# Kernel tuning notes

Measured on AMD Instinct MI355X. Metric: run time of the kernel, lower is better.

The kernel has to match this reference:

```python
import jax, jax.numpy as jnp
import numpy as np

B, T, L = 64, 256, 20
WV, WD = 100000, 300
CV, CD = 100, 100
PV, PD = 50, 100
NF, K = 100, 3
H = 256
D0 = WD + PD + NF        # 500, layer-0 LSTM input
D1 = 2 * H               # 512, later layers' input


def _lstm_dir(gx, mask, w_hh, reverse):
    # gx: [B,T,4H] precomputed input contribution + bias; mask: [B,T,1]
    if reverse:
        gx = gx[:, ::-1]
        mask = mask[:, ::-1]
    b, h = gx.shape[0], w_hh.shape[1]
    h0 = jnp.zeros((b, h), gx.dtype)

    def step(carry, xs):
        hp, cp = carry
        g_t, m_t = xs
        gates = g_t + hp @ w_hh.T
        i, f, g, o = jnp.split(gates, 4, axis=-1)
        i = jax.nn.sigmoid(i); f = jax.nn.sigmoid(f)
        o = jax.nn.sigmoid(o); g = jnp.tanh(g)
        c_new = f * cp + i * g
        h_new = o * jnp.tanh(c_new)
        hn = m_t * h_new + (1.0 - m_t) * hp   # masked step (pad positions keep state)
        cn = m_t * c_new + (1.0 - m_t) * cp
        return (hn, cn), hn

    _, hs = jax.lax.scan(step, (h0, h0), (gx.transpose(1, 0, 2), mask.transpose(1, 0, 2)))
    hs = hs.transpose(1, 0, 2)
    return hs[:, ::-1] if reverse else hs


def _bilstm_layer(x, mask, w_ih, w_hh, b):
    # w_ih: [2,4H,D], w_hh: [2,4H,H], b: [2,4H] (b_ih+b_hh combined)
    outs = []
    for d in range(2):
        gx = jnp.einsum('btd,gd->btg', x, w_ih[d]) + b[d]
        outs.append(_lstm_dir(gx, mask, w_hh[d], reverse=(d == 1)))
    return jnp.concatenate(outs, axis=-1)


def setup_inputs() -> dict:
    key = jax.random.key(0)
    ks = jax.random.split(key, 16)
    s = 0.05
    inp = {
        'input_word': jax.random.randint(ks[0], (B, T), 0, WV),
        'input_char': jax.random.randint(ks[1], (B, T, L), 0, CV),
        'input_pos': jax.random.randint(ks[2], (B, T), 0, PV),
        'mask': jnp.ones((B, T), jnp.float32),
        'emb_word': jax.random.normal(ks[3], (WV, WD), jnp.float32) * s,
        'emb_char': jax.random.normal(ks[4], (CV, CD), jnp.float32) * s,
        'emb_pos': jax.random.normal(ks[5], (PV, PD), jnp.float32) * s,
        'conv_w': jax.random.normal(ks[6], (NF, CD, K), jnp.float32) * s,
        'conv_b': jax.random.normal(ks[7], (NF,), jnp.float32) * s,
        'w_ih0': jax.random.normal(ks[8], (2, 4 * H, D0), jnp.float32) * s,
        'w_hh0': jax.random.normal(ks[9], (2, 4 * H, H), jnp.float32) * s,
        'b0': jax.random.normal(ks[10], (2, 4 * H), jnp.float32) * s,
        'w_ih1': jax.random.normal(ks[11], (2, 4 * H, D1), jnp.float32) * s,
        'w_hh1': jax.random.normal(ks[12], (2, 4 * H, H), jnp.float32) * s,
        'b1': jax.random.normal(ks[13], (2, 4 * H), jnp.float32) * s,
        'w_ih2': jax.random.normal(ks[14], (2, 4 * H, D1), jnp.float32) * s,
        'w_hh2': jax.random.normal(ks[15], (2, 4 * H, H), jnp.float32) * s,
        'b2': jax.random.normal(jax.random.fold_in(key, 99), (2, 4 * H), jnp.float32) * s,
    }
    return inp


def reference(input_word, input_char, input_pos, mask,
              emb_word, emb_char, emb_pos, conv_w, conv_b,
              w_ih0, w_hh0, b0, w_ih1, w_hh1, b1, w_ih2, w_hh2, b2):
    # dropout layers are identity in eval mode
    word = emb_word[input_word]                       # [B,T,WD]
    b, t, l = input_char.shape
    ch = emb_char[input_char].reshape(b * t, l, CD).transpose(0, 2, 1)  # [BT,CD,L]
    conv = jax.lax.conv_general_dilated(
        ch, conv_w, window_strides=(1,), padding=[(K - 1, K - 1)],
        dimension_numbers=('NCH', 'OIH', 'NCH')) + conv_b[None, :, None]
    ch = jnp.tanh(conv.max(axis=2)).reshape(b, t, NF)  # [B,T,NF]
    pos = emb_pos[input_pos]                           # [B,T,PD]
    x = jnp.concatenate([word, ch, pos], axis=-1)      # [B,T,D0]
    m = mask[..., None]
    x = _bilstm_layer(x, m, w_ih0, w_hh0, b0)
    x = _bilstm_layer(x, m, w_ih1, w_hh1, b1)
    x = _bilstm_layer(x, m, w_ih2, w_hh2, b2)
    return x                                           # [B,T,2H]
```

## Files before the change

kernel.cpp:

```cpp
#include <hip/hip_runtime.h>
#include <cstdint>
#include <cstddef>
#include <type_traits>
#include <utility>

typedef unsigned short u16;
typedef short short8 __attribute__((ext_vector_type(8)));
typedef __bf16 bf16x8 __attribute__((ext_vector_type(8)));
typedef float float4v __attribute__((ext_vector_type(4)));

__device__ __forceinline__ float bf2f(u16 u) {
  union { uint32_t i; float f; } v; v.i = ((uint32_t)u) << 16; return v.f;
}
__device__ __forceinline__ u16 f2bf(float f) {
  union { uint32_t i; float f; } v; v.f = f;
  uint32_t u = v.i;
  return (u16)((u + 0x7FFFu + ((u >> 16) & 1u)) >> 16);
}

__device__ __forceinline__ float fsig(float x) {
  float e = __expf(-x);
  return __builtin_amdgcn_rcpf(1.0f + e);
}
__device__ __forceinline__ float ftanh(float x) {
  float e = __expf(2.0f * x);
  return 1.0f - 2.0f * __builtin_amdgcn_rcpf(e + 1.0f);
}

__device__ __forceinline__ void bar_lgkm() {
  __builtin_amdgcn_sched_barrier(0);
  asm volatile("s_waitcnt lgkmcnt(0)" ::: "memory");
  __builtin_amdgcn_s_barrier();
  __builtin_amdgcn_sched_barrier(0);
}
__device__ __forceinline__ void bar_only() {
  __builtin_amdgcn_sched_barrier(0);
  __builtin_amdgcn_s_barrier();
  __builtin_amdgcn_sched_barrier(0);
}
__device__ __forceinline__ void bar_vm4() {
  __builtin_amdgcn_sched_barrier(0);
  asm volatile("s_waitcnt vmcnt(4) lgkmcnt(0)" ::: "memory");
  __builtin_amdgcn_s_barrier();
  __builtin_amdgcn_sched_barrier(0);
}

template <class V, class = void> struct MfmaTakesShort : std::false_type {};
template <class V>
struct MfmaTakesShort<V, std::void_t<decltype(__builtin_amdgcn_mfma_f32_16x16x32_bf16(
    std::declval<V>(), std::declval<V>(), std::declval<float4v>(), 0, 0, 0))>>
    : std::true_type {};

template <bool UseShort> struct MF {
  template <class V>
  static __device__ __forceinline__ float4v run(V a, V b, float4v c) {
    return __builtin_amdgcn_mfma_f32_16x16x32_bf16(a, b, c, 0, 0, 0);
  }
};
template <> struct MF<false> {
  template <class V>
  static __device__ __forceinline__ float4v run(V a, V b, float4v c) {
    return __builtin_amdgcn_mfma_f32_16x16x32_bf16(
        __builtin_bit_cast(bf16x8, a), __builtin_bit_cast(bf16x8, b), c, 0, 0, 0);
  }
};
__device__ __forceinline__ float4v mfma_bf16(short8 a, short8 b, float4v c) {
  return MF<MfmaTakesShort<short8>::value>::run(a, b, c);
}

__global__ void k_cvt_wih(const float* __restrict__ w, u16* __restrict__ o, int Kin) {
  int id = blockIdx.x * 256 + threadIdx.x;
  int n = id >> 9, k = id & 511;
  o[id] = (k < Kin) ? f2bf(w[(long)n * Kin + k]) : (u16)0;
}

__global__ void k_cvt_whh(const float* __restrict__ w, u16* __restrict__ o) {
  int id = blockIdx.x * 256 + threadIdx.x;
  o[id] = f2bf(w[id]);
}

__global__ void k_proj(const float* __restrict__ ec, const float* __restrict__ cw,
                       u16* __restrict__ proj) {
  int v = blockIdx.x, idx = threadIdx.x;
  if (idx >= 300) return;
  int k = idx / 100, nf = idx % 100;
  float s = 0.f;
  for (int cd = 0; cd < 100; cd++)
    s += ec[v * 100 + cd] * cw[(nf * 100 + cd) * 3 + k];
  proj[v * 300 + k * 100 + nf] = f2bf(s);
}

__global__ void k_embed(const int* __restrict__ iw, const int* __restrict__ ip,
                        const float* __restrict__ ew, const float* __restrict__ ep,
                        u16* __restrict__ x) {
  int row = blockIdx.x, j = threadIdx.x;
  u16 v;
  if (j < 300) v = f2bf(ew[(long)iw[row] * 300 + j]);
  else if (j < 400) return;
  else if (j < 500) v = f2bf(ep[ip[row] * 100 + (j - 400)]);
  else v = 0;
  x[row * 512 + j] = v;
}

__global__ __launch_bounds__(128) void k_charconv(const int* __restrict__ ic,
                                                  const u16* __restrict__ proj,
                                                  const float* __restrict__ cb,
                                                  u16* __restrict__ x) {
  __shared__ u16 pl[30000];
  __shared__ int ids[20];
  int tid = threadIdx.x;
  for (int i = tid; i < 15000; i += 128)
    ((uint32_t*)pl)[i] = ((const uint32_t*)proj)[i];
  float bias = (tid < 100) ? cb[tid] : 0.f;
  for (int r = 0; r < 16; r++) {
    int row = blockIdx.x * 16 + r;
    __syncthreads();
    if (tid < 20) ids[tid] = ic[row * 20 + tid];
    __syncthreads();
    if (tid < 100) {
      float mx = -1e30f;
      for (int p = 0; p < 22; p++) {
        float s = 0.f;
#pragma unroll
        for (int k = 0; k < 3; k++) {
          int q = p + k - 2;
          if (q >= 0 && q < 20) s += bf2f(pl[ids[q] * 300 + k * 100 + tid]);
        }
        mx = fmaxf(mx, s);
      }
      x[row * 512 + 300 + tid] = f2bf(ftanh(mx + bias));
    }
  }
}

template <bool GXF32>
__global__ __launch_bounds__(256) void k_gemm(const u16* __restrict__ A,
                                              const u16* __restrict__ Bm,
                                              const float* __restrict__ bias,
                                              void* __restrict__ Cv) {
  __shared__ u16 lA[128 * 64];
  __shared__ u16 lB[128 * 64];
  int tid = threadIdx.x;
  int w = tid >> 6, l = tid & 63, q = l >> 4, c16 = l & 15;
  int wm = w >> 1, wn = w & 1;
  int m0 = blockIdx.y * 128, n0 = blockIdx.x * 128;
  float4v acc[4][4];
#pragma unroll
  for (int i = 0; i < 4; i++)
#pragma unroll
    for (int j = 0; j < 4; j++) acc[i][j] = (float4v){0.f, 0.f, 0.f, 0.f};

  for (int kk = 0; kk < 512; kk += 64) {
    __syncthreads();
#pragma unroll
    for (int j = 0; j < 4; j++) {
      int idx = j * 256 + tid;
      int m = idx >> 3, k8 = (idx & 7) * 8;
      *(short8*)(lA + idx * 8) = *(const short8*)(A + (long)(m0 + m) * 512 + kk + k8);
      *(short8*)(lB + idx * 8) = *(const short8*)(Bm + (long)(n0 + m) * 512 + kk + k8);
    }
    __syncthreads();
#pragma unroll
    for (int kt = 0; kt < 2; kt++) {
      short8 af[4], bfv[4];
#pragma unroll
      for (int mt = 0; mt < 4; mt++)
        af[mt] = *(const short8*)(lA + (wm * 64 + mt * 16 + c16) * 64 + kt * 32 + q * 8);
#pragma unroll
      for (int nt = 0; nt < 4; nt++)
        bfv[nt] = *(const short8*)(lB + (wn * 64 + nt * 16 + c16) * 64 + kt * 32 + q * 8);
#pragma unroll
      for (int mt = 0; mt < 4; mt++)
#pragma unroll
        for (int nt = 0; nt < 4; nt++)
          acc[mt][nt] = mfma_bf16(af[mt], bfv[nt], acc[mt][nt]);
    }
  }
#pragma unroll
  for (int mt = 0; mt < 4; mt++)
#pragma unroll
    for (int nt = 0; nt < 4; nt++) {
      int ng = n0 + wn * 64 + nt * 16 + c16;
      float bv = bias[ng];
#pragma unroll
      for (int r = 0; r < 4; r++) {
        long mg = m0 + wm * 64 + mt * 16 + q * 4 + r;
        float val = acc[mt][nt][r] + bv;
        if constexpr (GXF32) ((float*)Cv)[mg * 2048 + ng] = val;
        else ((u16*)Cv)[mg * 2048 + ng] = f2bf(val);
      }
    }
}

template <bool GXF32, bool OUTF32>
__global__ __launch_bounds__(512, 2) void k_recur(
    const void* __restrict__ gxv, const u16* __restrict__ whh,
    const float* __restrict__ mask, void* __restrict__ outv,
    unsigned long long* __restrict__ hx, unsigned* __restrict__ flags) {
  __shared__ u16 hls[2][16 * 136];
  int tid = threadIdx.x;
  int w = tid >> 6, l = tid & 63, q = l >> 4, c16 = l & 15;
  int blk = blockIdx.x;
  int pair = blk & 7, half = blk >> 3;
  int bg = pair >> 1, d = pair & 1;
  int b0 = bg * 16;
  int ht = half * 8 + w;
  const u16* Wd = whh + d * (1024 * 256);

  for (int i = tid; i < 16 * 136; i += 512) hls[0][i] = 0;

  short8 Breg[32];
#pragma unroll
  for (int g = 0; g < 4; g++)
#pragma unroll
    for (int j = 0; j < 8; j++) {
      int ktg = (j < 4) ? (half * 4 + j) : ((half ^ 1) * 4 + (j - 4));
      Breg[g * 8 + j] =
          *(const short8*)(Wd + ((g * 16 + ht) * 16 + c16) * 256 + ktg * 32 + q * 8);
    }

  float c_[4] = {0.f, 0.f, 0.f, 0.f};
  unsigned hprev[2] = {0u, 0u};
  __syncthreads();

  const float* gxf = (const float*)gxv;
  const u16* gxh = (const u16*)gxv;
  float* outf = (float*)outv;
  u16* outh = (u16*)outv;

  int rb[4];
#pragma unroll
  for (int r = 0; r < 4; r++)
    rb[r] = (b0 + q * 4 + r) * 524288 + d * 1024 + ht * 16 + c16;
  const float* mrow = mask + (b0 + q * 4) * 256;

#pragma unroll 1
  for (int s = 0; s < 256; s++) {
    int t = d ? (255 - s) : s;
    const u16* hrd = hls[s & 1];
    u16* hwr = hls[(s & 1) ^ 1];

    short8 png[4];
    if (s > 0) {
      if (tid == 0) {
        unsigned idx = (unsigned)((s - 1) * 16 + pair * 2 + (half ^ 1));
        unsigned cnt = 0;
        while (__hip_atomic_load(&flags[idx], __ATOMIC_ACQUIRE,
                                 __HIP_MEMORY_SCOPE_AGENT) == 0u) {
          if (++cnt > 1000000u) break;
          __builtin_amdgcn_s_sleep(1);
        }
      }
      bar_only();
      const unsigned long long* ps =
          hx + ((size_t)(pair * 2 + ((s - 1) & 1)) * 2 + (half ^ 1)) * 512;
#pragma unroll
      for (int ktl = 0; ktl < 4; ktl++) {
        unsigned long long v0 = __hip_atomic_load(&ps[ktl * 128 + l * 2],
                                                  __ATOMIC_RELAXED,
                                                  __HIP_MEMORY_SCOPE_AGENT);
        unsigned long long v1 = __hip_atomic_load(&ps[ktl * 128 + l * 2 + 1],
                                                  __ATOMIC_RELAXED,
                                                  __HIP_MEMORY_SCOPE_AGENT);
        union { unsigned long long u[2]; short8 s8; } uu;
        uu.u[0] = v0; uu.u[1] = v1;
        png[ktl] = uu.s8;
      }
    }
    __builtin_amdgcn_sched_barrier(0);

    float m4[4];
#pragma unroll
    for (int r = 0; r < 4; r++) m4[r] = mrow[r * 256 + t];
    float gxc[16];
    if constexpr (GXF32) {
      const float* gxs = gxf + (size_t)t * 2048;
#pragma unroll
      for (int r = 0; r < 4; r++) {
        const float* p = gxs + rb[r];
#pragma unroll
        for (int g = 0; g < 4; g++) gxc[g * 4 + r] = p[g * 256];
      }
    } else {
      const u16* gxs = gxh + (size_t)t * 2048;
#pragma unroll
      for (int r = 0; r < 4; r++) {
        const u16* p = gxs + rb[r];
#pragma unroll
        for (int g = 0; g < 4; g++) gxc[g * 4 + r] = bf2f(p[g * 256]);
      }
    }
    __builtin_amdgcn_sched_barrier(0);

    float4v acc[4];
#pragma unroll
    for (int g = 0; g < 4; g++) acc[g] = (float4v){0.f, 0.f, 0.f, 0.f};
#pragma unroll
    for (int ktl = 0; ktl < 4; ktl++) {
      short8 a = *(const short8*)(hrd + c16 * 136 + ktl * 32 + q * 8);
#pragma unroll
      for (int g = 0; g < 4; g++)
        acc[g] = mfma_bf16(a, Breg[g * 8 + ktl], acc[g]);
    }

    if (s > 0) {
#pragma unroll
      for (int ktl = 0; ktl < 4; ktl++)
#pragma unroll
        for (int g = 0; g < 4; g++)
          acc[g] = mfma_bf16(png[ktl], Breg[g * 8 + 4 + ktl], acc[g]);
    }

    unsigned p0 = 0u, p1 = 0u;
    float hfv[4];
#pragma unroll
    for (int r = 0; r < 4; r++) {
      float mt = m4[r];
      float iv = fsig(acc[0][r] + gxc[0 + r]);
      float fv = fsig(acc[1][r] + gxc[4 + r]);
      float gv = ftanh(acc[2][r] + gxc[8 + r]);
      float ov = fsig(acc[3][r] + gxc[12 + r]);
      unsigned hpw = hprev[r >> 1];
      union { uint32_t i; float f; } hu;
      hu.i = (r & 1) ? (hpw & 0xFFFF0000u) : (hpw << 16);
      float hpo = hu.f;
      float cn = fv * c_[r] + iv * gv;
      float hn = ov * ftanh(cn);
      hn = mt * hn + (1.f - mt) * hpo;
      cn = mt * cn + (1.f - mt) * c_[r];
      c_[r] = cn;
      hfv[r] = hn;
      unsigned hb = (unsigned)f2bf(hn) << ((r & 1) * 16);
      if (r < 2) p0 |= hb; else p1 |= hb;
    }

    if (s < 255) {
#pragma unroll
      for (int r = 0; r < 4; r++) {
        u16 hb = (u16)(((r < 2) ? p0 : p1) >> ((r & 1) * 16));
        hwr[(q * 4 + r) * 136 + w * 16 + c16] = hb;
      }
      bar_lgkm();

      {
        int ktl2 = tid >> 7, ll = (tid >> 1) & 63, j = tid & 1;
        int qq = ll >> 4, cc = ll & 15;
        unsigned long long v =
            *(const unsigned long long*)(hwr + cc * 136 + ktl2 * 32 + qq * 8 + j * 4);
        __hip_atomic_store(
            &hx[((size_t)(pair * 2 + (s & 1)) * 2 + half) * 512 + tid], v,
            __ATOMIC_RELAXED, __HIP_MEMORY_SCOPE_AGENT);
      }
      __builtin_amdgcn_sched_barrier(0);
#pragma unroll
      for (int r = 0; r < 4; r++) {
        long oidx = ((long)((b0 + q * 4 + r) * 256 + t)) * 512 + d * 256 + ht * 16 + c16;
        if constexpr (OUTF32) outf[oidx] = hfv[r];
        else outh[oidx] = (u16)(((r < 2) ? p0 : p1) >> ((r & 1) * 16));
      }
      bar_vm4();
      if (tid == 0)
        __hip_atomic_store(&flags[s * 16 + pair * 2 + half], 1u, __ATOMIC_RELEASE,
                           __HIP_MEMORY_SCOPE_AGENT);
    } else {
#pragma unroll
      for (int r = 0; r < 4; r++) {
        long oidx = ((long)((b0 + q * 4 + r) * 256 + t)) * 512 + d * 256 + ht * 16 + c16;
        if constexpr (OUTF32) outf[oidx] = hfv[r];
        else outh[oidx] = (u16)(((r < 2) ? p0 : p1) >> ((r & 1) * 16));
      }
    }

    hprev[0] = p0; hprev[1] = p1;
  }
}

extern "C" void kernel_launch(void* const* d_in, const int* in_sizes, int n_in,
                              void* d_out, int out_size, void* d_ws, size_t ws_size,
                              hipStream_t stream) {
  const int* iw = (const int*)d_in[0];
  const int* ic = (const int*)d_in[1];
  const int* ip = (const int*)d_in[2];
  const float* mask = (const float*)d_in[3];
  const float* ew = (const float*)d_in[4];
  const float* ec = (const float*)d_in[5];
  const float* ep = (const float*)d_in[6];
  const float* cw = (const float*)d_in[7];
  const float* cb = (const float*)d_in[8];
  const float* wih[3] = {(const float*)d_in[9], (const float*)d_in[12], (const float*)d_in[15]};
  const float* whh[3] = {(const float*)d_in[10], (const float*)d_in[13], (const float*)d_in[16]};
  const float* bs[3] = {(const float*)d_in[11], (const float*)d_in[14], (const float*)d_in[17]};

  char* ws = (char*)d_ws;
  size_t szX0 = (size_t)16384 * 512 * 2;
  size_t szGXf = (size_t)16384 * 2048 * 4;
  size_t szWIH = (size_t)2048 * 512 * 2;
  size_t szWHH = (size_t)2 * 1024 * 256 * 2;
  size_t szPROJ = 60032;
  size_t szHX = (size_t)8 * 2 * 2 * 4096;
  size_t szFLG = (size_t)256 * 16 * 4;
  bool f32gx = ws_size >= szX0 + szGXf + szWIH + szWHH + szPROJ + szHX + szFLG;

  size_t off = 0;
  u16* X0 = (u16*)(ws + off); off += szX0;
  void* GX = (void*)(ws + off); off += f32gx ? szGXf : (szGXf / 2);
  u16* WIHB = (u16*)(ws + off); off += szWIH;
  u16* WHHB = (u16*)(ws + off); off += szWHH;
  u16* PROJ = (u16*)(ws + off); off += szPROJ;
  unsigned long long* HX = (unsigned long long*)(ws + off); off += szHX;
  unsigned* FLG = (unsigned*)(ws + off);
  u16* X1 = (u16*)d_out;

  hipLaunchKernelGGL(k_proj, dim3(100), dim3(320), 0, stream, ec, cw, PROJ);
  hipLaunchKernelGGL(k_embed, dim3(16384), dim3(512), 0, stream, iw, ip, ew, ep, X0);
  hipLaunchKernelGGL(k_charconv, dim3(1024), dim3(128), 0, stream, ic, PROJ, cb, X0);

  const u16* Xin[3] = {X0, X1, X0};
  void* Xout[3] = {(void*)X1, (void*)X0, d_out};
  int Kin[3] = {500, 512, 512};

  for (int lyr = 0; lyr < 3; lyr++) {
    hipLaunchKernelGGL(k_cvt_wih, dim3(4096), dim3(256), 0, stream, wih[lyr], WIHB, Kin[lyr]);
    hipLaunchKernelGGL(k_cvt_whh, dim3(2048), dim3(256), 0, stream, whh[lyr], WHHB);
    hipMemsetAsync(FLG, 0, szFLG, stream);
    if (f32gx) {
      hipLaunchKernelGGL((k_gemm<true>), dim3(16, 128), dim3(256), 0, stream,
                         Xin[lyr], WIHB, bs[lyr], GX);
      if (lyr < 2)
        hipLaunchKernelGGL((k_recur<true, false>), dim3(16), dim3(512), 0, stream,
                           GX, WHHB, mask, Xout[lyr], HX, FLG);
      else
        hipLaunchKernelGGL((k_recur<true, true>), dim3(16), dim3(512), 0, stream,
                           GX, WHHB, mask, Xout[lyr], HX, FLG);
    } else {
      hipLaunchKernelGGL((k_gemm<false>), dim3(16, 128), dim3(256), 0, stream,
                         Xin[lyr], WIHB, bs[lyr], GX);
      if (lyr < 2)
        hipLaunchKernelGGL((k_recur<false, false>), dim3(16), dim3(512), 0, stream,
                           GX, WHHB, mask, Xout[lyr], HX, FLG);
      else
        hipLaunchKernelGGL((k_recur<false, true>), dim3(16), dim3(512), 0, stream,
                           GX, WHHB, mask, Xout[lyr], HX, FLG);
    }
  }
}
```

Measured before the change: 2.737 ms.

## Transpose recurrent MFMA operands, prefetch next-step gates, and flatten cross-block handoff

```diff
diff --git a/kernel.cpp b/kernel.cpp
--- a/kernel.cpp
+++ b/kernel.cpp
@@ -25,24 +25,6 @@
 __device__ __forceinline__ float ftanh(float x) {
   float e = __expf(2.0f * x);
   return 1.0f - 2.0f * __builtin_amdgcn_rcpf(e + 1.0f);
-}
-
-__device__ __forceinline__ void bar_lgkm() {
-  __builtin_amdgcn_sched_barrier(0);
-  asm volatile("s_waitcnt lgkmcnt(0)" ::: "memory");
-  __builtin_amdgcn_s_barrier();
-  __builtin_amdgcn_sched_barrier(0);
-}
-__device__ __forceinline__ void bar_only() {
-  __builtin_amdgcn_sched_barrier(0);
-  __builtin_amdgcn_s_barrier();
-  __builtin_amdgcn_sched_barrier(0);
-}
-__device__ __forceinline__ void bar_vm4() {
-  __builtin_amdgcn_sched_barrier(0);
-  asm volatile("s_waitcnt vmcnt(4) lgkmcnt(0)" ::: "memory");
-  __builtin_amdgcn_s_barrier();
-  __builtin_amdgcn_sched_barrier(0);
 }
 
 template <class V, class = void> struct MfmaTakesShort : std::false_type {};
@@ -199,7 +181,10 @@
     unsigned long long* __restrict__ hx, unsigned* __restrict__ flags) {
   __shared__ u16 hls[2][16 * 136];
   int tid = threadIdx.x;
-  int w = tid >> 6, l = tid & 63, q = l >> 4, c16 = l & 15;
+  int w = tid >> 6, l = tid & 63;
+  int row = l & 15;
+  int cg = l >> 4;
+  int c4 = cg * 4;
   int blk = blockIdx.x;
   int pair = blk & 7, half = blk >> 3;
   int bg = pair >> 1, d = pair & 1;
@@ -216,11 +201,11 @@
     for (int j = 0; j < 8; j++) {
       int ktg = (j < 4) ? (half * 4 + j) : ((half ^ 1) * 4 + (j - 4));
       Breg[g * 8 + j] =
-          *(const short8*)(Wd + ((g * 16 + ht) * 16 + c16) * 256 + ktg * 32 + q * 8);
+          *(const short8*)(Wd + ((g * 16 + ht) * 16 + row) * 256 + ktg * 32 + cg * 8);
     }
 
   float c_[4] = {0.f, 0.f, 0.f, 0.f};
-  unsigned hprev[2] = {0u, 0u};
+  unsigned long long hp64 = 0ull;
   __syncthreads();
 
   const float* gxf = (const float*)gxv;
@@ -228,11 +213,26 @@
   float* outf = (float*)outv;
   u16* outh = (u16*)outv;
 
-  int rb[4];
-#pragma unroll
-  for (int r = 0; r < 4; r++)
-    rb[r] = (b0 + q * 4 + r) * 524288 + d * 1024 + ht * 16 + c16;
-  const float* mrow = mask + (b0 + q * 4) * 256;
+  int grow = b0 + row;
+  const float* mrowp = mask + grow * 256;
+  size_t gxbase = (size_t)grow * 524288 + d * 1024 + ht * 16 + c4;
+  long obase = ((long)grow * 256) * 512 + d * 256 + ht * 16 + c4;
+
+  using GxT = std::conditional_t<GXF32, float4v, unsigned long long>;
+  GxT gxc[4], gxn[4];
+  float mcur, mnxt;
+
+  {
+    int t0 = d ? 255 : 0;
+    mcur = mrowp[t0];
+#pragma unroll
+    for (int g = 0; g < 4; g++) {
+      if constexpr (GXF32)
+        gxc[g] = *(const float4v*)(gxf + gxbase + (size_t)t0 * 2048 + g * 256);
+      else
+        gxc[g] = *(const unsigned long long*)(gxh + gxbase + (size_t)t0 * 2048 + g * 256);
+    }
+  }
 
 #pragma unroll 1
   for (int s = 0; s < 256; s++) {
@@ -242,26 +242,23 @@
 
     short8 png[4];
     if (s > 0) {
-      if (tid == 0) {
-        unsigned idx = (unsigned)((s - 1) * 16 + pair * 2 + (half ^ 1));
-        unsigned cnt = 0;
-        while (__hip_atomic_load(&flags[idx], __ATOMIC_ACQUIRE,
-                                 __HIP_MEMORY_SCOPE_AGENT) == 0u) {
-          if (++cnt > 1000000u) break;
-          __builtin_amdgcn_s_sleep(1);
-        }
-      }
-      bar_only();
+      unsigned fidx = (unsigned)((s - 1) * 16 + pair * 2 + (half ^ 1));
+      unsigned cnt = 0;
+      while (__hip_atomic_load(&flags[fidx], __ATOMIC_RELAXED,
+                               __HIP_MEMORY_SCOPE_AGENT) == 0u) {
+        if (++cnt > 1000000u) break;
+        __builtin_amdgcn_s_sleep(1);
+      }
       const unsigned long long* ps =
           hx + ((size_t)(pair * 2 + ((s - 1) & 1)) * 2 + (half ^ 1)) * 512;
 #pragma unroll
       for (int ktl = 0; ktl < 4; ktl++) {
-        unsigned long long v0 = __hip_atomic_load(&ps[ktl * 128 + l * 2],
-                                                  __ATOMIC_RELAXED,
-                                                  __HIP_MEMORY_SCOPE_AGENT);
-        unsigned long long v1 = __hip_atomic_load(&ps[ktl * 128 + l * 2 + 1],
-                                                  __ATOMIC_RELAXED,
-                                                  __HIP_MEMORY_SCOPE_AGENT);
+        unsigned long long v0 = __hip_atomic_load(
+            &ps[(ktl * 8 + cg * 2 + 0) * 16 + row], __ATOMIC_RELAXED,
+            __HIP_MEMORY_SCOPE_AGENT);
+        unsigned long long v1 = __hip_atomic_load(
+            &ps[(ktl * 8 + cg * 2 + 1) * 16 + row], __ATOMIC_RELAXED,
+            __HIP_MEMORY_SCOPE_AGENT);
         union { unsigned long long u[2]; short8 s8; } uu;
         uu.u[0] = v0; uu.u[1] = v1;
         png[ktl] = uu.s8;
@@ -269,109 +266,92 @@
     }
     __builtin_amdgcn_sched_barrier(0);
 
-    float m4[4];
-#pragma unroll
-    for (int r = 0; r < 4; r++) m4[r] = mrow[r * 256 + t];
-    float gxc[16];
-    if constexpr (GXF32) {
-      const float* gxs = gxf + (size_t)t * 2048;
-#pragma unroll
-      for (int r = 0; r < 4; r++) {
-        const float* p = gxs + rb[r];
-#pragma unroll
-        for (int g = 0; g < 4; g++) gxc[g * 4 + r] = p[g * 256];
-      }
-    } else {
-      const u16* gxs = gxh + (size_t)t * 2048;
-#pragma unroll
-      for (int r = 0; r < 4; r++) {
-        const u16* p = gxs + rb[r];
-#pragma unroll
-        for (int g = 0; g < 4; g++) gxc[g * 4 + r] = bf2f(p[g * 256]);
-      }
-    }
-    __builtin_amdgcn_sched_barrier(0);
-
     float4v acc[4];
 #pragma unroll
     for (int g = 0; g < 4; g++) acc[g] = (float4v){0.f, 0.f, 0.f, 0.f};
 #pragma unroll
     for (int ktl = 0; ktl < 4; ktl++) {
-      short8 a = *(const short8*)(hrd + c16 * 136 + ktl * 32 + q * 8);
+      short8 b = *(const short8*)(hrd + row * 136 + ktl * 32 + cg * 8);
 #pragma unroll
       for (int g = 0; g < 4; g++)
-        acc[g] = mfma_bf16(a, Breg[g * 8 + ktl], acc[g]);
-    }
-
+        acc[g] = mfma_bf16(Breg[g * 8 + ktl], b, acc[g]);
+    }
     if (s > 0) {
 #pragma unroll
       for (int ktl = 0; ktl < 4; ktl++)
 #pragma unroll
         for (int g = 0; g < 4; g++)
-          acc[g] = mfma_bf16(png[ktl], Breg[g * 8 + 4 + ktl], acc[g]);
-    }
-
-    unsigned p0 = 0u, p1 = 0u;
-    float hfv[4];
+          acc[g] = mfma_bf16(Breg[g * 8 + 4 + ktl], png[ktl], acc[g]);
+    }
+
+    float mt = mcur, mo = 1.f - mcur;
+    float hnv[4];
+    unsigned long long hn64 = 0ull;
 #pragma unroll
     for (int r = 0; r < 4; r++) {
-      float mt = m4[r];
-      float iv = fsig(acc[0][r] + gxc[0 + r]);
-      float fv = fsig(acc[1][r] + gxc[4 + r]);
-      float gv = ftanh(acc[2][r] + gxc[8 + r]);
-      float ov = fsig(acc[3][r] + gxc[12 + r]);
-      unsigned hpw = hprev[r >> 1];
-      union { uint32_t i; float f; } hu;
-      hu.i = (r & 1) ? (hpw & 0xFFFF0000u) : (hpw << 16);
-      float hpo = hu.f;
+      float gi, gf, gg, go;
+      if constexpr (GXF32) {
+        gi = gxc[0][r]; gf = gxc[1][r]; gg = gxc[2][r]; go = gxc[3][r];
+      } else {
+        gi = bf2f((u16)(gxc[0] >> (r * 16)));
+        gf = bf2f((u16)(gxc[1] >> (r * 16)));
+        gg = bf2f((u16)(gxc[2] >> (r * 16)));
+        go = bf2f((u16)(gxc[3] >> (r * 16)));
+      }
+      float iv = fsig(acc[0][r] + gi);
+      float fv = fsig(acc[1][r] + gf);
+      float gv = ftanh(acc[2][r] + gg);
+      float ov = fsig(acc[3][r] + go);
+      float hpo = bf2f((u16)(hp64 >> (r * 16)));
       float cn = fv * c_[r] + iv * gv;
       float hn = ov * ftanh(cn);
-      hn = mt * hn + (1.f - mt) * hpo;
-      cn = mt * cn + (1.f - mt) * c_[r];
+      hn = mt * hn + mo * hpo;
+      cn = mt * cn + mo * c_[r];
       c_[r] = cn;
-      hfv[r] = hn;
-      unsigned hb = (unsigned)f2bf(hn) << ((r & 1) * 16);
-      if (r < 2) p0 |= hb; else p1 |= hb;
+      hnv[r] = hn;
+      hn64 |= ((unsigned long long)f2bf(hn)) << (r * 16);
     }
 
     if (s < 255) {
-#pragma unroll
-      for (int r = 0; r < 4; r++) {
-        u16 hb = (u16)(((r < 2) ? p0 : p1) >> ((r & 1) * 16));
-        hwr[(q * 4 + r) * 136 + w * 16 + c16] = hb;
-      }
-      bar_lgkm();
-
-      {
-        int ktl2 = tid >> 7, ll = (tid >> 1) & 63, j = tid & 1;
-        int qq = ll >> 4, cc = ll & 15;
-        unsigned long long v =
-            *(const unsigned long long*)(hwr + cc * 136 + ktl2 * 32 + qq * 8 + j * 4);
-        __hip_atomic_store(
-            &hx[((size_t)(pair * 2 + (s & 1)) * 2 + half) * 512 + tid], v,
-            __ATOMIC_RELAXED, __HIP_MEMORY_SCOPE_AGENT);
-      }
+      __hip_atomic_store(
+          &hx[((size_t)(pair * 2 + (s & 1)) * 2 + half) * 512 + (w * 4 + cg) * 16 + row],
+          hn64, __ATOMIC_RELAXED, __HIP_MEMORY_SCOPE_AGENT);
       __builtin_amdgcn_sched_barrier(0);
-#pragma unroll
-      for (int r = 0; r < 4; r++) {
-        long oidx = ((long)((b0 + q * 4 + r) * 256 + t)) * 512 + d * 256 + ht * 16 + c16;
-        if constexpr (OUTF32) outf[oidx] = hfv[r];
-        else outh[oidx] = (u16)(((r < 2) ? p0 : p1) >> ((r & 1) * 16));
-      }
-      bar_vm4();
+      *(unsigned long long*)(hwr + row * 136 + w * 16 + c4) = hn64;
+      if constexpr (OUTF32) {
+        float4v ov4 = {hnv[0], hnv[1], hnv[2], hnv[3]};
+        *(float4v*)(outf + obase + (long)t * 512) = ov4;
+      } else {
+        *(unsigned long long*)(outh + obase + (long)t * 512) = hn64;
+      }
+      int tn = d ? (254 - s) : (s + 1);
+      mnxt = mrowp[tn];
+#pragma unroll
+      for (int g = 0; g < 4; g++) {
+        if constexpr (GXF32)
+          gxn[g] = *(const float4v*)(gxf + gxbase + (size_t)tn * 2048 + g * 256);
+        else
+          gxn[g] = *(const unsigned long long*)(gxh + gxbase + (size_t)tn * 2048 + g * 256);
+      }
+      __builtin_amdgcn_sched_barrier(0);
+      asm volatile("s_waitcnt vmcnt(6) lgkmcnt(0)" ::: "memory");
+      __builtin_amdgcn_s_barrier();
+      __builtin_amdgcn_sched_barrier(0);
       if (tid == 0)
-        __hip_atomic_store(&flags[s * 16 + pair * 2 + half], 1u, __ATOMIC_RELEASE,
+        __hip_atomic_store(&flags[s * 16 + pair * 2 + half], 1u, __ATOMIC_RELAXED,
                            __HIP_MEMORY_SCOPE_AGENT);
+#pragma unroll
+      for (int g = 0; g < 4; g++) gxc[g] = gxn[g];
+      mcur = mnxt;
     } else {
-#pragma unroll
-      for (int r = 0; r < 4; r++) {
-        long oidx = ((long)((b0 + q * 4 + r) * 256 + t)) * 512 + d * 256 + ht * 16 + c16;
-        if constexpr (OUTF32) outf[oidx] = hfv[r];
-        else outh[oidx] = (u16)(((r < 2) ? p0 : p1) >> ((r & 1) * 16));
-      }
-    }
-
-    hprev[0] = p0; hprev[1] = p1;
+      if constexpr (OUTF32) {
+        float4v ov4 = {hnv[0], hnv[1], hnv[2], hnv[3]};
+        *(float4v*)(outf + obase + (long)t * 512) = ov4;
+      } else {
+        *(unsigned long long*)(outh + obase + (long)t * 512) = hn64;
+      }
+    }
+    hp64 = hn64;
   }
 }
 
```

Result: faster. 2.642 ms (-3.5%).
